# Performance work log

Hardware: AMD Instinct MI355X
Metric: run time of the kernel (lower is better)

Reference implementation:

```python
import jax, jax.numpy as jnp
import numpy as np

N_NODES, N_EDGES = 8, 8
NODE_FEAT, EDGE_FEAT = 4, 3
NODE_EMB, EDGE_EMB = 9, 8
N_LAYER = 3
N_QUBITS = NODE_EMB + EDGE_EMB + 2  # 19

H_GATE = (jnp.array([[1, 1], [1, -1]], jnp.complex64) / np.sqrt(2).astype(np.float32))
CNOT4 = jnp.asarray(np.array([[1, 0, 0, 0], [0, 1, 0, 0], [0, 0, 0, 1], [0, 0, 1, 0]],
                             np.complex64).reshape(2, 2, 2, 2))


def rx_mat(t):
    c = jnp.cos(0.5 * t).astype(jnp.complex64)
    s = (-1j) * jnp.sin(0.5 * t).astype(jnp.complex64)
    return jnp.stack([jnp.stack([c, s]), jnp.stack([s, c])])


def rz_mat(t):
    e = jnp.exp(-0.5j * t.astype(jnp.complex64))
    z = jnp.zeros((), jnp.complex64)
    return jnp.stack([jnp.stack([e, z]), jnp.stack([z, jnp.conj(e)])])


def apply_1q(psi, U, w):
    psi = jnp.tensordot(U, psi, axes=((1,), (w,)))
    return jnp.moveaxis(psi, 0, w)


def apply_cnot(psi, c, t):
    psi = jnp.tensordot(CNOT4, psi, axes=((2, 3), (c, t)))
    return jnp.moveaxis(psi, (0, 1), (c, t))


def gcn_conv(x, src, dst, W, b, n):
    # PyG GCNConv: add self-loops, symmetric D^-1/2 (A+I) D^-1/2 normalization
    h = x @ W  # (n, out)
    src2 = jnp.concatenate([src, jnp.arange(n)])
    dst2 = jnp.concatenate([dst, jnp.arange(n)])
    deg = jax.ops.segment_sum(jnp.ones(src2.shape[0], x.dtype), dst2, num_segments=n)
    dis = jnp.where(deg > 0, jax.lax.rsqrt(jnp.maximum(deg, 1e-12)), 0.0)
    coef = dis[src2] * dis[dst2]
    out = jax.ops.segment_sum(h[src2] * coef[:, None], dst2, num_segments=n)
    return out + b


def quantum_circuit(feats, qweights):
    psi = jnp.zeros((2,) * N_QUBITS, jnp.complex64).at[(0,) * N_QUBITS].set(1.0)
    # feature_map: Hadamards + BasicEntanglerLayers(1 layer, rotation=RZ)
    for q in range(N_QUBITS):
        psi = apply_1q(psi, H_GATE, q)
    for q in range(N_QUBITS):
        psi = apply_1q(psi, rz_mat(feats[q]), q)
    for q in range(N_QUBITS):
        psi = apply_cnot(psi, q, (q + 1) % N_QUBITS)
    # two ansatz blocks (weights first dim is 2), each with N_LAYER layers
    for i in range(2):
        w = qweights[i]  # (N_QUBITS, N_LAYER)
        for j in range(N_LAYER):
            for q in range(N_QUBITS):
                psi = apply_1q(psi, rx_mat(w[q, j]), q)
                psi = apply_1q(psi, rz_mat(w[q, j]), q)
            for q in range(N_QUBITS):
                psi = apply_cnot(psi, q, (q + 1) % N_QUBITS)
    pr = jnp.sum(jnp.abs(psi.reshape(2, -1)) ** 2, axis=1)  # marginal of qubit 0
    return (pr[0] - pr[1]).astype(jnp.float32)  # <Z_0>


def setup_inputs() -> dict:
    key = jax.random.key(0)
    ks = jax.random.split(key, 20)
    inp = {
        "edge_index": jax.random.randint(ks[0], (2, N_EDGES), 0, N_NODES),
        "state": jax.random.normal(ks[1], (N_NODES, NODE_FEAT), jnp.float32),
        "mass": jax.random.normal(ks[2], (N_EDGES,), jnp.float32),
        "spin": jax.random.normal(ks[3], (N_EDGES,), jnp.float32),
        "charge": jax.random.normal(ks[4], (N_EDGES,), jnp.float32),
        "p_norm": jax.random.normal(ks[5], (1,), jnp.float32),
        "theta": jax.random.normal(ks[6], (1,), jnp.float32),
        "scattering": jax.random.normal(ks[7], (1,), jnp.float32),
        "gcn_node_w": jax.random.normal(ks[8], (NODE_FEAT, 1), jnp.float32) * 0.3,
        "gcn_node_b": jnp.zeros((1,), jnp.float32),
        "gcn_edge_w": jax.random.normal(ks[9], (EDGE_FEAT, 1), jnp.float32) * 0.3,
        "gcn_edge_b": jnp.zeros((1,), jnp.float32),
        "node_w": jax.random.normal(ks[10], (N_NODES, NODE_EMB), jnp.float32) * 0.3,
        "node_b": jnp.zeros((NODE_EMB,), jnp.float32),
        "edge_w": jax.random.normal(ks[11], (N_EDGES, EDGE_EMB), jnp.float32) * 0.3,
        "edge_b": jnp.zeros((EDGE_EMB,), jnp.float32),
        "qweights": jax.random.normal(ks[12], (2, N_QUBITS, N_LAYER), jnp.float32) * 0.1,
    }
    return inp


def reference(edge_index, state, mass, spin, charge, p_norm, theta, scattering,
              gcn_node_w, gcn_node_b, gcn_edge_w, gcn_edge_b,
              node_w, node_b, edge_w, edge_b, qweights):
    src, dst = edge_index[0], edge_index[1]
    x_edges = jnp.stack([mass, spin, charge], axis=1)  # (E, 3)
    x1 = gcn_conv(state, src, dst, gcn_node_w, gcn_node_b, N_NODES).reshape(-1)
    x1 = x1 @ node_w + node_b  # (NODE_EMB,)
    x2 = gcn_conv(x_edges, src, dst, gcn_edge_w, gcn_edge_b, N_EDGES).reshape(-1)
    x2 = x2 @ edge_w + edge_b  # (EDGE_EMB,)
    feats = jnp.concatenate([x1, x2, p_norm.reshape(-1), theta.reshape(-1)])  # (N_QUBITS,)
    return quantum_circuit(feats, qweights)
```

## Files before the change

kernel.cpp:

```cpp
#include <hip/hip_runtime.h>

#define NQ 19
#define SZ (1u << NQ)

__global__ __launch_bounds__(128)
void k_prep(const int* __restrict__ ei, const float* __restrict__ state,
            const float* __restrict__ mass, const float* __restrict__ spin,
            const float* __restrict__ charge, const float* __restrict__ p_norm,
            const float* __restrict__ theta,
            const float* __restrict__ gnw, const float* __restrict__ gnb,
            const float* __restrict__ gew, const float* __restrict__ geb,
            const float* __restrict__ nw, const float* __restrict__ nb,
            const float* __restrict__ ew, const float* __restrict__ eb,
            const float* __restrict__ qw,
            float2* __restrict__ G, float2* __restrict__ E0,
            float2* __restrict__ E1)
{
    __shared__ double feats[NQ];
    int tid = threadIdx.x;
    if (tid == 0) {
        double deg[8], dis[8], h[8], o1[8], he[8], o2[8];
        for (int v = 0; v < 8; ++v) deg[v] = 1.0;
        for (int e = 0; e < 8; ++e) deg[ei[8 + e]] += 1.0;
        for (int v = 0; v < 8; ++v) dis[v] = 1.0 / sqrt(deg[v]);
        for (int v = 0; v < 8; ++v) {
            double s = 0.0;
            for (int k = 0; k < 4; ++k) s += (double)state[v * 4 + k] * (double)gnw[k];
            h[v] = s;
        }
        for (int v = 0; v < 8; ++v) o1[v] = h[v] * dis[v] * dis[v] + (double)gnb[0];
        for (int e = 0; e < 8; ++e) {
            int s = ei[e], d = ei[8 + e];
            o1[d] += h[s] * dis[s] * dis[d];
        }
        for (int j = 0; j < 9; ++j) {
            double a = (double)nb[j];
            for (int v = 0; v < 8; ++v) a += o1[v] * (double)nw[v * 9 + j];
            feats[j] = a;
        }
        for (int e = 0; e < 8; ++e)
            he[e] = (double)mass[e] * (double)gew[0] + (double)spin[e] * (double)gew[1]
                  + (double)charge[e] * (double)gew[2];
        for (int v = 0; v < 8; ++v) o2[v] = he[v] * dis[v] * dis[v] + (double)geb[0];
        for (int e = 0; e < 8; ++e) {
            int s = ei[e], d = ei[8 + e];
            o2[d] += he[s] * dis[s] * dis[d];
        }
        for (int j = 0; j < 8; ++j) {
            double a = (double)eb[j];
            for (int v = 0; v < 8; ++v) a += o2[v] * (double)ew[v * 8 + j];
            feats[9 + j] = a;
        }
        feats[17] = (double)p_norm[0];
        feats[18] = (double)theta[0];
    }
    __syncthreads();
    for (int g = tid; g < 6 * NQ; g += blockDim.x) {
        int l = g / NQ, q = g % NQ;
        int i = l / 3, j = l % 3;
        double t = (double)qw[i * (NQ * 3) + q * 3 + j];
        double c = cos(0.5 * t), s = sin(0.5 * t);
        int k = 18 - q;
        float2* Ug = &G[(l * NQ + k) * 4];
        Ug[0] = make_float2((float)(c * c), (float)(-s * c));
        Ug[1] = make_float2((float)(-s * s), (float)(-c * s));
        Ug[2] = make_float2((float)(s * s), (float)(-c * s));
        Ug[3] = make_float2((float)(c * c), (float)(s * c));
    }
    double S = 0.0;
    for (int q = 0; q < NQ; ++q) S += feats[q];
    for (int m = tid; m < 1024; m += blockDim.x) {
        double a = -0.5 * S;
        for (int k = 0; k < 10; ++k)
            if ((m >> k) & 1) a += feats[18 - k];
        double sp, cp;
        sincos(a, &sp, &cp);
        E0[m] = make_float2((float)cp, (float)sp);
    }
    const double amp = 1.0 / sqrt((double)SZ);
    for (int m = tid; m < 512; m += blockDim.x) {
        double a = 0.0;
        for (int k = 0; k < 9; ++k)
            if ((m >> k) & 1) a += feats[8 - k];
        double sp, cp;
        sincos(a, &sp, &cp);
        E1[m] = make_float2((float)(amp * cp), (float)(amp * sp));
    }
}

__device__ __forceinline__ unsigned pinv(unsigned c)
{
    unsigned y = (c ^ (c >> 1)) & 0x1FFFFu;
    unsigned c0 = c & 1u, c17 = (c >> 17) & 1u, c18 = (c >> 18) & 1u;
    return y | ((c0 ^ c17 ^ c18) << 17) | ((c0 ^ c18) << 18);
}

__device__ __forceinline__ unsigned padl(unsigned l) { return l + 2u * (l >> 3); }

__device__ __forceinline__ void bfly(float2& a, float2& b,
                                     float2 u00, float2 u01,
                                     float2 u10, float2 u11)
{
    float2 na, nb;
    na.x = u00.x * a.x - u00.y * a.y + u01.x * b.x - u01.y * b.y;
    na.y = u00.x * a.y + u00.y * a.x + u01.x * b.y + u01.y * b.x;
    nb.x = u10.x * a.x - u10.y * a.y + u11.x * b.x - u11.y * b.y;
    nb.y = u10.x * a.y + u10.y * a.x + u11.x * b.y + u11.y * b.x;
    a = na;
    b = nb;
}

__device__ __forceinline__ void apply_gates(float2 r[8], const float2* __restrict__ Gl,
                                            int ampbit0, int jbit0, int n)
{
    #pragma unroll
    for (int k = 0; k < n; ++k) {
        const float2 u00 = Gl[(ampbit0 + k) * 4 + 0];
        const float2 u01 = Gl[(ampbit0 + k) * 4 + 1];
        const float2 u10 = Gl[(ampbit0 + k) * 4 + 2];
        const float2 u11 = Gl[(ampbit0 + k) * 4 + 3];
        const int m = 1 << (jbit0 + k);
        #pragma unroll
        for (int j = 0; j < 8; ++j)
            if (!(j & m)) bfly(r[j], r[j | m], u00, u01, u10, u11);
    }
}

__global__ __launch_bounds__(256)
void k_layerA(const float2* __restrict__ in, float2* __restrict__ out,
              const float2* __restrict__ G, int layer,
              const float2* __restrict__ E0, const float2* __restrict__ E1,
              int first)
{
    __shared__ __align__(16) float2 lds0[2560];
    __shared__ __align__(16) float2 lds1[2560];
    const unsigned t = threadIdx.x;
    const unsigned base = blockIdx.x << 11;
    const float2* Gl = G + layer * NQ * 4;
    float2 r[8];

    if (first) {
        #pragma unroll
        for (int j = 0; j < 8; ++j) {
            unsigned b = pinv(base | (t * 8u + (unsigned)j));
            float2 e0 = E0[b & 1023u], e1 = E1[b >> 10];
            r[j] = make_float2(e0.x * e1.x - e0.y * e1.y,
                               e0.x * e1.y + e0.y * e1.x);
        }
    } else {
        #pragma unroll
        for (int j = 0; j < 8; ++j)
            r[j] = in[pinv(base | (t * 8u + (unsigned)j))];
    }
    apply_gates(r, Gl, 0, 0, 3);

    #pragma unroll
    for (int jh = 0; jh < 4; ++jh) {
        unsigned l = t * 8u + (unsigned)jh * 2u;
        *reinterpret_cast<float4*>(&lds0[padl(l)]) =
            make_float4(r[2 * jh].x, r[2 * jh].y, r[2 * jh + 1].x, r[2 * jh + 1].y);
    }
    __syncthreads();
    #pragma unroll
    for (int j = 0; j < 8; ++j)
        r[j] = lds0[padl((t & 7u) | ((unsigned)j << 3) | ((t >> 3) << 6))];
    apply_gates(r, Gl, 3, 0, 3);

    #pragma unroll
    for (int j = 0; j < 8; ++j)
        lds1[padl((t & 7u) | ((unsigned)j << 3) | ((t >> 3) << 6))] = r[j];
    __syncthreads();
    #pragma unroll
    for (int j = 0; j < 8; ++j)
        r[j] = lds1[padl((t & 63u) | ((unsigned)j << 6) | ((t >> 6) << 9))];
    apply_gates(r, Gl, 6, 0, 3);

    #pragma unroll
    for (int j = 0; j < 8; ++j)
        lds0[padl((t & 63u) | ((unsigned)j << 6) | ((t >> 6) << 9))] = r[j];
    __syncthreads();
    #pragma unroll
    for (int jh = 0; jh < 4; ++jh) {
        float4 v = *reinterpret_cast<const float4*>(
            &lds0[padl((t << 1) | ((unsigned)jh << 9))]);
        r[2 * jh]     = make_float2(v.x, v.y);
        r[2 * jh + 1] = make_float2(v.z, v.w);
    }
    apply_gates(r, Gl, 9, 1, 2);

    #pragma unroll
    for (int jh = 0; jh < 4; ++jh) {
        unsigned l = (t << 1) | ((unsigned)jh << 9);
        *reinterpret_cast<float4*>(&out[base | l]) =
            make_float4(r[2 * jh].x, r[2 * jh].y, r[2 * jh + 1].x, r[2 * jh + 1].y);
    }
}

__global__ __launch_bounds__(256)
void k_layerB(float2* __restrict__ buf, const float2* __restrict__ G, int layer,
              int do_reduce, double* __restrict__ partial)
{
    __shared__ __align__(16) float2 lds0[2560];
    __shared__ __align__(16) float2 lds1[2560];
    const unsigned t = threadIdx.x;
    const unsigned blk = blockIdx.x;
    const float2* Gl = G + layer * NQ * 4;
    float2 r[8];

    #pragma unroll
    for (int j = 0; j < 8; ++j) {
        unsigned g = (blk << 3) | (t & 7u) | ((unsigned)j << 11) | ((t >> 3) << 14);
        r[j] = buf[g];
    }
    apply_gates(r, Gl, 11, 0, 3);

    #pragma unroll
    for (int j = 0; j < 8; ++j)
        lds0[padl((t & 7u) | ((unsigned)j << 3) | ((t >> 3) << 6))] = r[j];
    __syncthreads();
    #pragma unroll
    for (int j = 0; j < 8; ++j)
        r[j] = lds0[padl((t & 63u) | ((unsigned)j << 6) | ((t >> 6) << 9))];
    apply_gates(r, Gl, 14, 0, 3);

    #pragma unroll
    for (int j = 0; j < 8; ++j)
        lds1[padl((t & 63u) | ((unsigned)j << 6) | ((t >> 6) << 9))] = r[j];
    __syncthreads();
    #pragma unroll
    for (int jh = 0; jh < 4; ++jh) {
        float4 v = *reinterpret_cast<const float4*>(
            &lds1[padl((t << 1) | ((unsigned)jh << 9))]);
        r[2 * jh]     = make_float2(v.x, v.y);
        r[2 * jh + 1] = make_float2(v.z, v.w);
    }
    apply_gates(r, Gl, 17, 1, 2);

    if (do_reduce) {
        __shared__ double sm[256];
        double acc = 0.0;
        #pragma unroll
        for (int jh = 0; jh < 4; ++jh) {
            unsigned l0 = (t << 1) | ((unsigned)jh << 9);
            unsigned g0 = (blk << 3) | (l0 & 7u) | ((l0 >> 3) << 11);
            float2 a = r[2 * jh], b = r[2 * jh + 1];
            double w0 = (double)a.x * a.x + (double)a.y * a.y;
            double w1 = (double)b.x * b.x + (double)b.y * b.y;
            double d = w0 - w1;
            acc += (__popc(g0 & 0x3FFFFu) & 1) ? -d : d;
        }
        sm[t] = acc;
        __syncthreads();
        for (int st = 128; st > 0; st >>= 1) {
            if ((int)t < st) sm[t] += sm[t + st];
            __syncthreads();
        }
        if (t == 0) partial[blk] = sm[0];
    } else {
        #pragma unroll
        for (int jh = 0; jh < 4; ++jh) {
            unsigned l = (t << 1) | ((unsigned)jh << 9);
            unsigned g = (blk << 3) | (l & 7u) | ((l >> 3) << 11);
            *reinterpret_cast<float4*>(&buf[g]) =
                make_float4(r[2 * jh].x, r[2 * jh].y, r[2 * jh + 1].x, r[2 * jh + 1].y);
        }
    }
}

__global__ __launch_bounds__(256)
void k_final(const double* __restrict__ partial, float* __restrict__ out)
{
    __shared__ double sm[256];
    sm[threadIdx.x] = partial[threadIdx.x];
    __syncthreads();
    for (int st = 128; st > 0; st >>= 1) {
        if ((int)threadIdx.x < st) sm[threadIdx.x] += sm[threadIdx.x + st];
        __syncthreads();
    }
    if (threadIdx.x == 0) out[0] = (float)sm[0];
}

extern "C" void kernel_launch(void* const* d_in, const int* in_sizes, int n_in,
                              void* d_out, int out_size, void* d_ws, size_t ws_size,
                              hipStream_t stream)
{
    const int*   ei      = (const int*)d_in[0];
    const float* state   = (const float*)d_in[1];
    const float* mass    = (const float*)d_in[2];
    const float* spin    = (const float*)d_in[3];
    const float* charge  = (const float*)d_in[4];
    const float* p_norm  = (const float*)d_in[5];
    const float* theta   = (const float*)d_in[6];
    const float* gnw     = (const float*)d_in[8];
    const float* gnb     = (const float*)d_in[9];
    const float* gew     = (const float*)d_in[10];
    const float* geb     = (const float*)d_in[11];
    const float* nw      = (const float*)d_in[12];
    const float* nb      = (const float*)d_in[13];
    const float* ew      = (const float*)d_in[14];
    const float* eb      = (const float*)d_in[15];
    const float* qw      = (const float*)d_in[16];

    char* ws = (char*)d_ws;
    float2* G       = (float2*)(ws);
    float2* E0      = (float2*)(ws + 4096);
    float2* E1      = (float2*)(ws + 12288);
    double* partial = (double*)(ws + 16384);
    float2* buf0    = (float2*)(ws + 32768);
    float2* buf1    = buf0 + SZ;

    k_prep<<<1, 128, 0, stream>>>(ei, state, mass, spin, charge, p_norm, theta,
                                  gnw, gnb, gew, geb, nw, nb, ew, eb, qw,
                                  G, E0, E1);

    float2* bufs[2] = {buf0, buf1};
    for (int l = 0; l < 6; ++l) {
        float2* in  = bufs[l & 1];
        float2* out = bufs[(l & 1) ^ 1];
        k_layerA<<<256, 256, 0, stream>>>(in, out, G, l, E0, E1, l == 0);
        k_layerB<<<256, 256, 0, stream>>>(out, G, l, l == 5, partial);
    }
    k_final<<<1, 256, 0, stream>>>(partial, (float*)d_out);
}
```

Measured before the change: 98.99 us.

## Split state-vector passes into 1024-amplitude tiles over 512 blocks with staged loads

Each layer pass now processes 1024 amplitudes per block with 4 per thread, using 512 blocks instead of 256 and radix-4 stages through two smaller LDS buffers. PassA stages the permuted input (or the E0/E1 product factors) through shared memory with contiguous float4 global loads, instead of gathering scattered elements with pinv indices. The aim is more blocks in flight to fill the GPU's compute units and more coalesced global reads. In exchange there are more LDS shuffle rounds and barriers per amplitude, and passB now uses scalar global loads and stores with a stride-2 pattern.

Result: slower. 124.3 us (+25.5%).

```diff
diff --git a/kernel.cpp b/kernel.cpp
--- a/kernel.cpp
+++ b/kernel.cpp
@@ -110,7 +110,7 @@
     b = nb;
 }
 
-__device__ __forceinline__ void apply_gates(float2 r[8], const float2* __restrict__ Gl,
+__device__ __forceinline__ void apply_gates(float2 r[4], const float2* __restrict__ Gl,
                                             int ampbit0, int jbit0, int n)
 {
     #pragma unroll
@@ -121,133 +121,172 @@
         const float2 u11 = Gl[(ampbit0 + k) * 4 + 3];
         const int m = 1 << (jbit0 + k);
         #pragma unroll
-        for (int j = 0; j < 8; ++j)
+        for (int j = 0; j < 4; ++j)
             if (!(j & m)) bfly(r[j], r[j | m], u00, u01, u10, u11);
     }
 }
 
 __global__ __launch_bounds__(256)
-void k_layerA(const float2* __restrict__ in, float2* __restrict__ out,
-              const float2* __restrict__ G, int layer,
-              const float2* __restrict__ E0, const float2* __restrict__ E1,
-              int first)
-{
-    __shared__ __align__(16) float2 lds0[2560];
-    __shared__ __align__(16) float2 lds1[2560];
+void k_passA(const float2* __restrict__ in, float2* __restrict__ out,
+             const float2* __restrict__ G, int layer,
+             const float2* __restrict__ E0, const float2* __restrict__ E1,
+             int first)
+{
+    __shared__ __align__(16) float2 Sstage[2560];
+    __shared__ __align__(16) float2 X0[1280];
+    __shared__ __align__(16) float2 X1[1280];
     const unsigned t = threadIdx.x;
-    const unsigned base = blockIdx.x << 11;
+    const unsigned base = blockIdx.x << 10;
     const float2* Gl = G + layer * NQ * 4;
-    float2 r[8];
+    float2 r[4];
 
     if (first) {
         #pragma unroll
-        for (int j = 0; j < 8; ++j) {
-            unsigned b = pinv(base | (t * 8u + (unsigned)j));
-            float2 e0 = E0[b & 1023u], e1 = E1[b >> 10];
+        for (int k = 0; k < 2; ++k) {
+            unsigned i = ((unsigned)k << 9) | (t << 1);
+            float4 v = *reinterpret_cast<const float4*>(&E0[i]);
+            *reinterpret_cast<float4*>(&Sstage[padl(i)]) = v;
+        }
+        {
+            unsigned i = t << 1;
+            float4 v = *reinterpret_cast<const float4*>(&E1[i]);
+            *reinterpret_cast<float4*>(&Sstage[padl(1024u + i)]) = v;
+        }
+    } else {
+        unsigned src0 = pinv(base) & ~1023u;
+        unsigned src1 = pinv(base | 1u) & ~1023u;
+        #pragma unroll
+        for (int k = 0; k < 4; ++k) {
+            unsigned i = ((unsigned)k << 9) | (t << 1);
+            unsigned g = (i >= 1024u) ? (src1 + (i - 1024u)) : (src0 + i);
+            float4 v = *reinterpret_cast<const float4*>(&in[g]);
+            *reinterpret_cast<float4*>(&Sstage[padl(i)]) = v;
+        }
+    }
+    __syncthreads();
+
+    #pragma unroll
+    for (int j = 0; j < 4; ++j) {
+        unsigned l = (t << 2) | (unsigned)j;
+        unsigned c = base | l;
+        unsigned b = pinv(c);
+        if (first) {
+            float2 e0 = Sstage[padl(b & 1023u)];
+            float2 e1 = Sstage[padl(1024u + (b >> 10))];
             r[j] = make_float2(e0.x * e1.x - e0.y * e1.y,
                                e0.x * e1.y + e0.y * e1.x);
-        }
-    } else {
-        #pragma unroll
-        for (int j = 0; j < 8; ++j)
-            r[j] = in[pinv(base | (t * 8u + (unsigned)j))];
-    }
-    apply_gates(r, Gl, 0, 0, 3);
-
-    #pragma unroll
-    for (int jh = 0; jh < 4; ++jh) {
-        unsigned l = t * 8u + (unsigned)jh * 2u;
-        *reinterpret_cast<float4*>(&lds0[padl(l)]) =
+        } else {
+            r[j] = Sstage[padl(((l & 1u) << 10) | (b & 1023u))];
+        }
+    }
+    apply_gates(r, Gl, 0, 0, 2);
+
+    #pragma unroll
+    for (int jh = 0; jh < 2; ++jh)
+        *reinterpret_cast<float4*>(&X0[padl((t << 2) | ((unsigned)jh << 1))]) =
             make_float4(r[2 * jh].x, r[2 * jh].y, r[2 * jh + 1].x, r[2 * jh + 1].y);
-    }
-    __syncthreads();
-    #pragma unroll
-    for (int j = 0; j < 8; ++j)
-        r[j] = lds0[padl((t & 7u) | ((unsigned)j << 3) | ((t >> 3) << 6))];
-    apply_gates(r, Gl, 3, 0, 3);
-
-    #pragma unroll
-    for (int j = 0; j < 8; ++j)
-        lds1[padl((t & 7u) | ((unsigned)j << 3) | ((t >> 3) << 6))] = r[j];
-    __syncthreads();
-    #pragma unroll
-    for (int j = 0; j < 8; ++j)
-        r[j] = lds1[padl((t & 63u) | ((unsigned)j << 6) | ((t >> 6) << 9))];
-    apply_gates(r, Gl, 6, 0, 3);
-
-    #pragma unroll
-    for (int j = 0; j < 8; ++j)
-        lds0[padl((t & 63u) | ((unsigned)j << 6) | ((t >> 6) << 9))] = r[j];
-    __syncthreads();
-    #pragma unroll
-    for (int jh = 0; jh < 4; ++jh) {
-        float4 v = *reinterpret_cast<const float4*>(
-            &lds0[padl((t << 1) | ((unsigned)jh << 9))]);
-        r[2 * jh]     = make_float2(v.x, v.y);
-        r[2 * jh + 1] = make_float2(v.z, v.w);
-    }
-    apply_gates(r, Gl, 9, 1, 2);
-
-    #pragma unroll
-    for (int jh = 0; jh < 4; ++jh) {
-        unsigned l = (t << 1) | ((unsigned)jh << 9);
-        *reinterpret_cast<float4*>(&out[base | l]) =
-            make_float4(r[2 * jh].x, r[2 * jh].y, r[2 * jh + 1].x, r[2 * jh + 1].y);
-    }
+    __syncthreads();
+    #pragma unroll
+    for (int j = 0; j < 4; ++j)
+        r[j] = X0[padl((t & 3u) | ((unsigned)j << 2) | ((t >> 2) << 4))];
+    apply_gates(r, Gl, 2, 0, 2);
+
+    #pragma unroll
+    for (int j = 0; j < 4; ++j)
+        X1[padl((t & 3u) | ((unsigned)j << 2) | ((t >> 2) << 4))] = r[j];
+    __syncthreads();
+    #pragma unroll
+    for (int j = 0; j < 4; ++j)
+        r[j] = X1[padl((t & 15u) | ((unsigned)j << 4) | ((t >> 4) << 6))];
+    apply_gates(r, Gl, 4, 0, 2);
+
+    #pragma unroll
+    for (int j = 0; j < 4; ++j)
+        X0[padl((t & 15u) | ((unsigned)j << 4) | ((t >> 4) << 6))] = r[j];
+    __syncthreads();
+    #pragma unroll
+    for (int j = 0; j < 4; ++j)
+        r[j] = X0[padl((t & 63u) | ((unsigned)j << 6) | ((t >> 6) << 8))];
+    apply_gates(r, Gl, 6, 0, 2);
+
+    #pragma unroll
+    for (int j = 0; j < 4; ++j)
+        X1[padl((t & 63u) | ((unsigned)j << 6) | ((t >> 6) << 8))] = r[j];
+    __syncthreads();
+    #pragma unroll
+    for (int j = 0; j < 4; ++j)
+        r[j] = X1[padl(t | ((unsigned)j << 8))];
+    apply_gates(r, Gl, 8, 0, 2);
+
+    #pragma unroll
+    for (int j = 0; j < 4; ++j)
+        out[base | t | ((unsigned)j << 8)] = r[j];
 }
 
 __global__ __launch_bounds__(256)
-void k_layerB(float2* __restrict__ buf, const float2* __restrict__ G, int layer,
-              int do_reduce, double* __restrict__ partial)
-{
-    __shared__ __align__(16) float2 lds0[2560];
-    __shared__ __align__(16) float2 lds1[2560];
+void k_passB(float2* __restrict__ buf, const float2* __restrict__ G, int layer,
+             int do_reduce, double* __restrict__ partial)
+{
+    __shared__ __align__(16) float2 X0[1280];
+    __shared__ __align__(16) float2 X1[1280];
+    __shared__ double sm[256];
     const unsigned t = threadIdx.x;
     const unsigned blk = blockIdx.x;
     const float2* Gl = G + layer * NQ * 4;
-    float2 r[8];
-
-    #pragma unroll
-    for (int j = 0; j < 8; ++j) {
-        unsigned g = (blk << 3) | (t & 7u) | ((unsigned)j << 11) | ((t >> 3) << 14);
-        r[j] = buf[g];
-    }
-    apply_gates(r, Gl, 11, 0, 3);
-
-    #pragma unroll
-    for (int j = 0; j < 8; ++j)
-        lds0[padl((t & 7u) | ((unsigned)j << 3) | ((t >> 3) << 6))] = r[j];
-    __syncthreads();
-    #pragma unroll
-    for (int j = 0; j < 8; ++j)
-        r[j] = lds0[padl((t & 63u) | ((unsigned)j << 6) | ((t >> 6) << 9))];
-    apply_gates(r, Gl, 14, 0, 3);
-
-    #pragma unroll
-    for (int j = 0; j < 8; ++j)
-        lds1[padl((t & 63u) | ((unsigned)j << 6) | ((t >> 6) << 9))] = r[j];
-    __syncthreads();
-    #pragma unroll
-    for (int jh = 0; jh < 4; ++jh) {
-        float4 v = *reinterpret_cast<const float4*>(
-            &lds1[padl((t << 1) | ((unsigned)jh << 9))]);
-        r[2 * jh]     = make_float2(v.x, v.y);
-        r[2 * jh + 1] = make_float2(v.z, v.w);
-    }
-    apply_gates(r, Gl, 17, 1, 2);
+    float2 r[4];
+
+    #pragma unroll
+    for (int j = 0; j < 4; ++j) {
+        unsigned c = (t & 1u) | (blk << 1) | ((unsigned)j << 10) | ((t >> 1) << 12);
+        r[j] = buf[c];
+    }
+    apply_gates(r, Gl, 10, 0, 2);
+
+    #pragma unroll
+    for (int j = 0; j < 4; ++j)
+        X0[padl((t & 1u) | ((unsigned)j << 1) | ((t >> 1) << 3))] = r[j];
+    __syncthreads();
+    #pragma unroll
+    for (int j = 0; j < 4; ++j)
+        r[j] = X0[padl((t & 7u) | ((unsigned)j << 3) | ((t >> 3) << 5))];
+    apply_gates(r, Gl, 12, 0, 2);
+
+    #pragma unroll
+    for (int j = 0; j < 4; ++j)
+        X1[padl((t & 7u) | ((unsigned)j << 3) | ((t >> 3) << 5))] = r[j];
+    __syncthreads();
+    #pragma unroll
+    for (int j = 0; j < 4; ++j)
+        r[j] = X1[padl((t & 31u) | ((unsigned)j << 5) | ((t >> 5) << 7))];
+    apply_gates(r, Gl, 14, 0, 2);
+
+    #pragma unroll
+    for (int j = 0; j < 4; ++j)
+        X0[padl((t & 31u) | ((unsigned)j << 5) | ((t >> 5) << 7))] = r[j];
+    __syncthreads();
+    #pragma unroll
+    for (int j = 0; j < 4; ++j)
+        r[j] = X0[padl((t & 127u) | ((unsigned)j << 7) | ((t >> 7) << 9))];
+    apply_gates(r, Gl, 16, 0, 2);
+
+    #pragma unroll
+    for (int j = 0; j < 4; ++j)
+        X1[padl((t & 127u) | ((unsigned)j << 7) | ((t >> 7) << 9))] = r[j];
+    __syncthreads();
+    #pragma unroll
+    for (int j = 0; j < 4; ++j)
+        r[j] = X1[padl(t | ((unsigned)j << 8))];
+    apply_gates(r, Gl, 18, 1, 1);
 
     if (do_reduce) {
-        __shared__ double sm[256];
         double acc = 0.0;
         #pragma unroll
-        for (int jh = 0; jh < 4; ++jh) {
-            unsigned l0 = (t << 1) | ((unsigned)jh << 9);
-            unsigned g0 = (blk << 3) | (l0 & 7u) | ((l0 >> 3) << 11);
-            float2 a = r[2 * jh], b = r[2 * jh + 1];
-            double w0 = (double)a.x * a.x + (double)a.y * a.y;
-            double w1 = (double)b.x * b.x + (double)b.y * b.y;
-            double d = w0 - w1;
-            acc += (__popc(g0 & 0x3FFFFu) & 1) ? -d : d;
+        for (int j = 0; j < 4; ++j) {
+            unsigned l = t | ((unsigned)j << 8);
+            unsigned c = (l & 1u) | (blk << 1) | ((l >> 1) << 10);
+            float2 v = r[j];
+            double w = (double)v.x * v.x + (double)v.y * v.y;
+            acc += (__popc(c & 0x3FFFFu) & 1) ? -w : w;
         }
         sm[t] = acc;
         __syncthreads();
@@ -258,11 +297,10 @@
         if (t == 0) partial[blk] = sm[0];
     } else {
         #pragma unroll
-        for (int jh = 0; jh < 4; ++jh) {
-            unsigned l = (t << 1) | ((unsigned)jh << 9);
-            unsigned g = (blk << 3) | (l & 7u) | ((l >> 3) << 11);
-            *reinterpret_cast<float4*>(&buf[g]) =
-                make_float4(r[2 * jh].x, r[2 * jh].y, r[2 * jh + 1].x, r[2 * jh + 1].y);
+        for (int j = 0; j < 4; ++j) {
+            unsigned l = t | ((unsigned)j << 8);
+            unsigned c = (l & 1u) | (blk << 1) | ((l >> 1) << 10);
+            buf[c] = r[j];
         }
     }
 }
@@ -271,7 +309,7 @@
 void k_final(const double* __restrict__ partial, float* __restrict__ out)
 {
     __shared__ double sm[256];
-    sm[threadIdx.x] = partial[threadIdx.x];
+    sm[threadIdx.x] = partial[threadIdx.x] + partial[threadIdx.x + 256];
     __syncthreads();
     for (int st = 128; st > 0; st >>= 1) {
         if ((int)threadIdx.x < st) sm[threadIdx.x] += sm[threadIdx.x + st];
@@ -317,8 +355,8 @@
     for (int l = 0; l < 6; ++l) {
         float2* in  = bufs[l & 1];
         float2* out = bufs[(l & 1) ^ 1];
-        k_layerA<<<256, 256, 0, stream>>>(in, out, G, l, E0, E1, l == 0);
-        k_layerB<<<256, 256, 0, stream>>>(out, G, l, l == 5, partial);
+        k_passA<<<512, 256, 0, stream>>>(in, out, G, l, E0, E1, l == 0);
+        k_passB<<<512, 256, 0, stream>>>(out, G, l, l == 5, partial);
     }
     k_final<<<1, 256, 0, stream>>>(partial, (float*)d_out);
 }
```
